# Kernel tuning notes

Measured on AMD Instinct MI355X. Metric: run time of the kernel, lower is better.

## Reference

```python
import jax, jax.numpy as jnp
import numpy as np

B, N, NIN = 32, 128, 64
MSG_HID, MSG_OUT, N_HID, N_OUT = 256, 64, 256, 64
E = N * (N - 1)  # fully connected, no self loops


def setup_inputs() -> dict:
    key = jax.random.key(0)
    ks = jax.random.split(key, 12)

    # one-hot incidence matrices (NRI convention)
    off = np.ones((N, N), dtype=np.float32) - np.eye(N, dtype=np.float32)
    recv_idx, send_idx = np.where(off)
    eye = np.eye(N, dtype=np.float32)
    rel_rec = jnp.asarray(eye[recv_idx])    # [E, N]
    rel_send = jnp.asarray(eye[send_idx])   # [E, N]

    s = 0.05
    inp = {
        "inputs": jax.random.normal(ks[0], (B, N, NIN), jnp.float32),
        "rel_rec": rel_rec,
        "rel_send": rel_send,
        "rel_types": jax.random.uniform(ks[1], (B, E, 2), jnp.float32),
        "msg_fc1_w": jax.random.normal(ks[2], (MSG_HID, 2 * NIN), jnp.float32) * s,
        "msg_fc1_b": jnp.zeros((MSG_HID,), jnp.float32),
        "msg_fc2_w": jax.random.normal(ks[3], (MSG_OUT, MSG_HID), jnp.float32) * s,
        "msg_fc2_b": jnp.zeros((MSG_OUT,), jnp.float32),
        "out_fc1_w": jax.random.normal(ks[4], (N_HID, MSG_OUT), jnp.float32) * s,
        "out_fc1_b": jnp.zeros((N_HID,), jnp.float32),
        "out_fc2_w": jax.random.normal(ks[5], (N_HID, N_HID), jnp.float32) * s,
        "out_fc2_b": jnp.zeros((N_HID,), jnp.float32),
        "out_fc3_w": jax.random.normal(ks[6], (N_OUT, N_HID), jnp.float32) * s,
        "out_fc3_b": jnp.zeros((N_OUT,), jnp.float32),
    }
    return inp


def reference(inputs, rel_rec, rel_send, rel_types,
              msg_fc1_w, msg_fc1_b, msg_fc2_w, msg_fc2_b,
              out_fc1_w, out_fc1_b, out_fc2_w, out_fc2_b,
              out_fc3_w, out_fc3_b):
    # node2edge: gather sender / receiver node features via one-hot matmul
    senders = jnp.einsum('en,bnf->bef', rel_send, inputs)    # [B,E,NIN]
    receivers = jnp.einsum('en,bnf->bef', rel_rec, inputs)   # [B,E,NIN]
    pre_msg = jnp.concatenate([senders, receivers], axis=-1)  # [B,E,2*NIN]

    all_msgs = jnp.zeros(pre_msg.shape[:2] + (MSG_OUT,), pre_msg.dtype)
    for i in range(2):  # edge-type loop (shared weights, as in the original)
        msg = jax.nn.relu(pre_msg @ msg_fc1_w.T + msg_fc1_b)
        msg = jax.nn.relu(msg @ msg_fc2_w.T + msg_fc2_b)
        all_msgs = all_msgs + msg * rel_types[:, :, i:i + 1]

    # edge2node: scatter-add messages to receiving nodes
    agg_msgs = jnp.einsum('bem,en->bnm', all_msgs, rel_rec)   # [B,N,MSG_OUT]

    pred = jax.nn.relu(agg_msgs @ out_fc1_w.T + out_fc1_b)
    pred = jax.nn.relu(pred @ out_fc2_w.T + out_fc2_b)
    pred = pred @ out_fc3_w.T + out_fc3_b                      # [B,N,N_OUT]
    return pred
```

## Files before the change

kernel.cpp:

```cpp
#include <hip/hip_runtime.h>

#define BB 32
#define NN_ 128
#define NIN 64
#define MH 256
#define MO 64
#define NH 256
#define NO 64
#define EDGES 16256

typedef _Float16 half8 __attribute__((ext_vector_type(8)));
typedef _Float16 half2t __attribute__((ext_vector_type(2)));
typedef __attribute__((ext_vector_type(4))) float f32x4;


static __device__ __forceinline__ unsigned short f2h(float f) {
    return __builtin_bit_cast(unsigned short, (_Float16)f);
}

static __device__ __forceinline__ half8 pack8h(float4 f0, float4 f1) {
    uint4 u;
    u.x = __builtin_bit_cast(unsigned, __builtin_amdgcn_cvt_pkrtz(f0.x, f0.y));
    u.y = __builtin_bit_cast(unsigned, __builtin_amdgcn_cvt_pkrtz(f0.z, f0.w));
    u.z = __builtin_bit_cast(unsigned, __builtin_amdgcn_cvt_pkrtz(f1.x, f1.y));
    u.w = __builtin_bit_cast(unsigned, __builtin_amdgcn_cvt_pkrtz(f1.z, f1.w));
    return __builtin_bit_cast(half8, u);
}

static __device__ __forceinline__ half8 addrelu(uint4 s, uint4 p) {
    half8 a = __builtin_bit_cast(half8, s) + __builtin_bit_cast(half8, p);
    half8 z = {};
    return __builtin_elementwise_max(a, z);
}

__global__ __launch_bounds__(256) void prep_kernel(
    const float* __restrict__ x, const float* __restrict__ W1,
    const float* __restrict__ b1, const float* __restrict__ W2,
    const float* __restrict__ O1, const float* __restrict__ O2,
    const float* __restrict__ O3,
    unsigned short* __restrict__ psb, unsigned short* __restrict__ prb,
    unsigned short* __restrict__ w2b, unsigned short* __restrict__ o1b,
    unsigned short* __restrict__ o2b, unsigned short* __restrict__ o3b)
{
    int blk = blockIdx.x;
    int t = threadIdx.x;
    if (blk < 256) {
        int row0 = blk << 4;
        int b = blk >> 3;
        int w = t >> 6, lane = t & 63, ml = lane & 15, q = lane >> 4;

        half8 aX[2];
        #pragma unroll
        for (int s = 0; s < 2; ++s) {
            const float* base = x + (size_t)(row0 + ml) * NIN + s * 32 + q * 8;
            aX[s] = pack8h(*(const float4*)base, *(const float4*)(base + 4));
        }

        #pragma unroll
        for (int half = 0; half < 2; ++half) {
            #pragma unroll
            for (int nt = 0; nt < 4; ++nt) {
                int col = w * 64 + nt * 16 + ml;
                const float* wrow = W1 + (size_t)col * (2 * NIN) + half * 64 + q * 8;
                f32x4 acc = (f32x4){0.f, 0.f, 0.f, 0.f};
                #pragma unroll
                for (int s = 0; s < 2; ++s) {
                    half8 bw = pack8h(*(const float4*)(wrow + 32 * s),
                                      *(const float4*)(wrow + 32 * s + 4));
                    acc = __builtin_amdgcn_mfma_f32_16x16x32_f16(aX[s], bw, acc, 0, 0, 0);
                }
                if (half == 0) {
                    #pragma unroll
                    for (int reg = 0; reg < 4; ++reg) {
                        int n = (row0 + q * 4 + reg) & 127;
                        psb[((size_t)(b * 32 + (col >> 3)) * NN_ + n) * 8 + (col & 7)]
                            = f2h(acc[reg]);
                    }
                } else {
                    float bv = b1[col];
                    #pragma unroll
                    for (int reg = 0; reg < 4; ++reg) {
                        int n = (row0 + q * 4 + reg) & 127;
                        prb[((size_t)(b * NN_) + n) * MH + col] = f2h(acc[reg] + bv);
                    }
                }
            }
        }
    } else if (blk < 320) {
        int i = ((blk - 256) << 8) + t;
        int kc4 = i >> 9, rem = i & 511;
        int n = rem >> 3, k7 = i & 7;
        w2b[i] = f2h(W2[n * MH + kc4 * 8 + k7]);
    } else {
        int i = ((blk - 320) << 8) + t;
        if (i < 16384)       o1b[i]         = f2h(O1[i]);
        else if (i < 81920)  o2b[i - 16384] = f2h(O2[i - 16384]);
        else                 o3b[i - 81920] = f2h(O3[i - 81920]);
    }
}

__global__ __launch_bounds__(256, 3) void edge_kernel(
    const float* __restrict__ rt, const float* __restrict__ b2,
    const unsigned short* __restrict__ psb, const unsigned short* __restrict__ prb,
    const unsigned short* __restrict__ w2b, float* __restrict__ agg)
{
    int blk = blockIdx.x;
    int b = blk >> 6;
    int r0 = (blk & 63) << 1;
    int tid = threadIdx.x;
    int w = tid >> 6, lane = tid & 63, ml = lane & 15, q = lane >> 4;

    __shared__ float rtw_lds[2][128];
    __shared__ float red[2][4][64];
    {
        int rr = tid >> 7, s = tid & 127;
        int r = r0 + rr;
        float v = 0.f;
        if (s != r) {
            int e = r * 127 + s - (s > r ? 1 : 0);
            const float* p = rt + ((size_t)(b * EDGES + e)) * 2;
            v = p[0] + p[1];
        }
        rtw_lds[rr][s] = v;
    }
    __syncthreads();

    int slot0 = 32 * w + ml;
    int slot1 = slot0 + 16;

    const uint4* ps4 = (const uint4*)psb + (size_t)b * (32 * NN_);
    const uint4* pr4_0 = (const uint4*)(prb + ((size_t)(b * NN_ + r0)) * MH);
    const uint4* pr4_1 = (const uint4*)(prb + ((size_t)(b * NN_ + r0 + 1)) * MH);
    const uint4* w24 = (const uint4*)w2b;

    f32x4 acc[2][2][4];
    #pragma unroll
    for (int rr = 0; rr < 2; ++rr)
        #pragma unroll
        for (int mt = 0; mt < 2; ++mt)
            #pragma unroll
            for (int nt = 0; nt < 4; ++nt)
                acc[rr][mt][nt] = (f32x4){0.f, 0.f, 0.f, 0.f};

    #pragma unroll
    for (int kc = 0; kc < 8; ++kc) {
        int kc4 = 4 * kc + q;
        uint4 us0 = ps4[kc4 * NN_ + slot0];
        uint4 us1 = ps4[kc4 * NN_ + slot1];
        uint4 up0 = pr4_0[kc4];
        uint4 up1 = pr4_1[kc4];

        half8 a00 = addrelu(us0, up0);
        half8 a01 = addrelu(us1, up0);
        half8 a10 = addrelu(us0, up1);
        half8 a11 = addrelu(us1, up1);

        #pragma unroll
        for (int nt = 0; nt < 4; ++nt) {
            half8 bw = __builtin_bit_cast(half8, w24[kc4 * 64 + 16 * nt + ml]);
            acc[0][0][nt] = __builtin_amdgcn_mfma_f32_16x16x32_f16(a00, bw, acc[0][0][nt], 0, 0, 0);
            acc[0][1][nt] = __builtin_amdgcn_mfma_f32_16x16x32_f16(a01, bw, acc[0][1][nt], 0, 0, 0);
            acc[1][0][nt] = __builtin_amdgcn_mfma_f32_16x16x32_f16(a10, bw, acc[1][0][nt], 0, 0, 0);
            acc[1][1][nt] = __builtin_amdgcn_mfma_f32_16x16x32_f16(a11, bw, acc[1][1][nt], 0, 0, 0);
        }
    }

    float b2c[4];
    #pragma unroll
    for (int nt = 0; nt < 4; ++nt) b2c[nt] = b2[16 * nt + ml];

    #pragma unroll
    for (int rr = 0; rr < 2; ++rr) {
        float colsum[4] = {0.f, 0.f, 0.f, 0.f};
        #pragma unroll
        for (int mt = 0; mt < 2; ++mt) {
            int slotbase = 32 * w + 16 * mt + 4 * q;
            #pragma unroll
            for (int reg = 0; reg < 4; ++reg) {
                float rw = rtw_lds[rr][slotbase + reg];
                #pragma unroll
                for (int nt = 0; nt < 4; ++nt)
                    colsum[nt] += fmaxf(acc[rr][mt][nt][reg] + b2c[nt], 0.f) * rw;
            }
        }
        #pragma unroll
        for (int nt = 0; nt < 4; ++nt) {
            colsum[nt] += __shfl_xor(colsum[nt], 16);
            colsum[nt] += __shfl_xor(colsum[nt], 32);
        }
        if (lane < 16) {
            #pragma unroll
            for (int nt = 0; nt < 4; ++nt) red[rr][w][16 * nt + ml] = colsum[nt];
        }
    }
    __syncthreads();
    if (tid < 128) {
        int rr = tid >> 6, o = tid & 63;
        agg[((size_t)(b * NN_ + r0 + rr)) * MO + o] =
            red[rr][0][o] + red[rr][1][o] + red[rr][2][o] + red[rr][3][o];
    }
}

__global__ __launch_bounds__(256) void node_kernel(
    const float* __restrict__ agg,
    const unsigned short* __restrict__ O1b, const float* __restrict__ b1o,
    const unsigned short* __restrict__ O2b, const float* __restrict__ b2o,
    const unsigned short* __restrict__ O3b, const float* __restrict__ b3o,
    float* __restrict__ out)
{
    int tid = threadIdx.x;
    int w = tid >> 6, lane = tid & 63, ml = lane & 15, q = lane >> 4;
    int row0 = blockIdx.x << 4;

    __shared__ unsigned short h1L[16][264];
    __shared__ unsigned short h2L[16][264];

    half8 aA[2];
    #pragma unroll
    for (int s = 0; s < 2; ++s) {
        const float* base = agg + (size_t)(row0 + ml) * MO + 32 * s + q * 8;
        aA[s] = pack8h(*(const float4*)base, *(const float4*)(base + 4));
    }

    #pragma unroll
    for (int nt = 0; nt < 4; ++nt) {
        int ntg = w * 4 + nt;
        f32x4 acc = (f32x4){0.f, 0.f, 0.f, 0.f};
        #pragma unroll
        for (int s = 0; s < 2; ++s) {
            half8 bw = *(const half8*)(O1b + (size_t)(ntg * 16 + ml) * 64 + 32 * s + q * 8);
            acc = __builtin_amdgcn_mfma_f32_16x16x32_f16(aA[s], bw, acc, 0, 0, 0);
        }
        float bv = b1o[ntg * 16 + ml];
        #pragma unroll
        for (int reg = 0; reg < 4; ++reg)
            h1L[q * 4 + reg][ntg * 16 + ml] = f2h(fmaxf(acc[reg] + bv, 0.f));
    }
    __syncthreads();

    half8 aH[8];
    #pragma unroll
    for (int ks = 0; ks < 8; ++ks)
        aH[ks] = *(const half8*)&h1L[ml][32 * ks + q * 8];
    #pragma unroll
    for (int nt = 0; nt < 4; ++nt) {
        int ntg = w * 4 + nt;
        const unsigned short* wrow = O2b + (size_t)(ntg * 16 + ml) * NH + q * 8;
        f32x4 acc = (f32x4){0.f, 0.f, 0.f, 0.f};
        #pragma unroll
        for (int ks = 0; ks < 8; ++ks) {
            half8 bw = *(const half8*)(wrow + 32 * ks);
            acc = __builtin_amdgcn_mfma_f32_16x16x32_f16(aH[ks], bw, acc, 0, 0, 0);
        }
        float bv = b2o[ntg * 16 + ml];
        #pragma unroll
        for (int reg = 0; reg < 4; ++reg)
            h2L[q * 4 + reg][ntg * 16 + ml] = f2h(fmaxf(acc[reg] + bv, 0.f));
    }
    __syncthreads();

    #pragma unroll
    for (int ks = 0; ks < 8; ++ks)
        aH[ks] = *(const half8*)&h2L[ml][32 * ks + q * 8];
    {
        const unsigned short* wrow = O3b + (size_t)(w * 16 + ml) * NH + q * 8;
        f32x4 acc = (f32x4){0.f, 0.f, 0.f, 0.f};
        #pragma unroll
        for (int ks = 0; ks < 8; ++ks) {
            half8 bw = *(const half8*)(wrow + 32 * ks);
            acc = __builtin_amdgcn_mfma_f32_16x16x32_f16(aH[ks], bw, acc, 0, 0, 0);
        }
        float bv = b3o[w * 16 + ml];
        #pragma unroll
        for (int reg = 0; reg < 4; ++reg)
            out[(size_t)(row0 + q * 4 + reg) * NO + w * 16 + ml] = acc[reg] + bv;
    }
}

extern "C" void kernel_launch(void* const* d_in, const int* in_sizes, int n_in,
                              void* d_out, int out_size, void* d_ws, size_t ws_size,
                              hipStream_t stream) {
    const float* x   = (const float*)d_in[0];
    const float* rt  = (const float*)d_in[3];
    const float* W1  = (const float*)d_in[4];
    const float* b1  = (const float*)d_in[5];
    const float* W2  = (const float*)d_in[6];
    const float* b2  = (const float*)d_in[7];
    const float* O1  = (const float*)d_in[8];
    const float* b1o = (const float*)d_in[9];
    const float* O2  = (const float*)d_in[10];
    const float* b2o = (const float*)d_in[11];
    const float* O3  = (const float*)d_in[12];
    const float* b3o = (const float*)d_in[13];

    float* ws  = (float*)d_ws;
    unsigned short* psb = (unsigned short*)ws;
    unsigned short* prb = (unsigned short*)(ws + 524288);
    unsigned short* w2b = (unsigned short*)(ws + 1048576);
    float* agg = ws + 1056768;
    unsigned short* o1b = (unsigned short*)(ws + 1318912);
    unsigned short* o2b = (unsigned short*)(ws + 1327104);
    unsigned short* o3b = (unsigned short*)(ws + 1359872);
    float* out = (float*)d_out;

    hipLaunchKernelGGL(prep_kernel, dim3(704), dim3(256), 0, stream,
                       x, W1, b1, W2, O1, O2, O3, psb, prb, w2b, o1b, o2b, o3b);
    hipLaunchKernelGGL(edge_kernel, dim3(2048), dim3(256), 0, stream,
                       rt, b2, psb, prb, w2b, agg);
    hipLaunchKernelGGL(node_kernel, dim3(256), dim3(256), 0, stream,
                       agg, o1b, b1o, o2b, b2o, o3b, b3o, out);
}
```

Baseline: 128.4 us.

## Fuse edge message kernel with node MLP kernel via LDS aggregation

Merges the edge kernel and the node MLP kernel into one launch. Each 512-thread block handles 8 receiver nodes in two teams over two iterations and keeps the aggregated messages in LDS instead of writing them to global memory. It then runs the three-layer node MLP on a zero-padded 16-row tile. This removes one kernel launch and the agg global round trip, but leaves only 512 blocks and wastes half of the node-MLP MFMA work on padding rows.

Result: slower. 256.1 us (+99.5%).

```diff
diff --git a/kernel.cpp b/kernel.cpp
--- a/kernel.cpp
+++ b/kernel.cpp
@@ -10,7 +10,6 @@
 #define EDGES 16256
 
 typedef _Float16 half8 __attribute__((ext_vector_type(8)));
-typedef _Float16 half2t __attribute__((ext_vector_type(2)));
 typedef __attribute__((ext_vector_type(4))) float f32x4;
 
 
@@ -99,136 +98,149 @@
     }
 }
 
-__global__ __launch_bounds__(256, 3) void edge_kernel(
+__global__ __launch_bounds__(512, 4) void edge_node_kernel(
     const float* __restrict__ rt, const float* __restrict__ b2,
     const unsigned short* __restrict__ psb, const unsigned short* __restrict__ prb,
-    const unsigned short* __restrict__ w2b, float* __restrict__ agg)
+    const unsigned short* __restrict__ w2b,
+    const unsigned short* __restrict__ o1b, const float* __restrict__ b1o,
+    const unsigned short* __restrict__ o2b, const float* __restrict__ b2o,
+    const unsigned short* __restrict__ o3b, const float* __restrict__ b3o,
+    float* __restrict__ out)
 {
     int blk = blockIdx.x;
-    int b = blk >> 6;
-    int r0 = (blk & 63) << 1;
-    int tid = threadIdx.x;
-    int w = tid >> 6, lane = tid & 63, ml = lane & 15, q = lane >> 4;
-
-    __shared__ float rtw_lds[2][128];
-    __shared__ float red[2][4][64];
-    {
-        int rr = tid >> 7, s = tid & 127;
-        int r = r0 + rr;
-        float v = 0.f;
-        if (s != r) {
-            int e = r * 127 + s - (s > r ? 1 : 0);
-            const float* p = rt + ((size_t)(b * EDGES + e)) * 2;
-            v = p[0] + p[1];
-        }
-        rtw_lds[rr][s] = v;
-    }
-    __syncthreads();
-
-    int slot0 = 32 * w + ml;
-    int slot1 = slot0 + 16;
+    int t = threadIdx.x;
+    int team = t >> 8;
+    int tl = t & 255;
+    int w = tl >> 6;
+    int lane = t & 63;
+    int ml = lane & 15, q = lane >> 4;
+
+    int b = blk >> 4;
+    int rbase = (blk & 15) << 3;
+
+    __shared__ float rtw_lds[2][2][128];
+    __shared__ float red[2][2][4][64];
+    __shared__ float aggL[16][68];
+    __shared__ unsigned short h1L[16][264];
+    __shared__ unsigned short h2L[16][264];
+
+    aggL[8 + (t >> 6)][lane] = 0.f;
+
+    float b2c[4];
+    #pragma unroll
+    for (int nt = 0; nt < 4; ++nt) b2c[nt] = b2[16 * nt + ml];
 
     const uint4* ps4 = (const uint4*)psb + (size_t)b * (32 * NN_);
-    const uint4* pr4_0 = (const uint4*)(prb + ((size_t)(b * NN_ + r0)) * MH);
-    const uint4* pr4_1 = (const uint4*)(prb + ((size_t)(b * NN_ + r0 + 1)) * MH);
     const uint4* w24 = (const uint4*)w2b;
 
-    f32x4 acc[2][2][4];
-    #pragma unroll
-    for (int rr = 0; rr < 2; ++rr)
-        #pragma unroll
-        for (int mt = 0; mt < 2; ++mt)
-            #pragma unroll
-            for (int nt = 0; nt < 4; ++nt)
-                acc[rr][mt][nt] = (f32x4){0.f, 0.f, 0.f, 0.f};
-
-    #pragma unroll
-    for (int kc = 0; kc < 8; ++kc) {
-        int kc4 = 4 * kc + q;
-        uint4 us0 = ps4[kc4 * NN_ + slot0];
-        uint4 us1 = ps4[kc4 * NN_ + slot1];
-        uint4 up0 = pr4_0[kc4];
-        uint4 up1 = pr4_1[kc4];
-
-        half8 a00 = addrelu(us0, up0);
-        half8 a01 = addrelu(us1, up0);
-        half8 a10 = addrelu(us0, up1);
-        half8 a11 = addrelu(us1, up1);
-
-        #pragma unroll
-        for (int nt = 0; nt < 4; ++nt) {
-            half8 bw = __builtin_bit_cast(half8, w24[kc4 * 64 + 16 * nt + ml]);
-            acc[0][0][nt] = __builtin_amdgcn_mfma_f32_16x16x32_f16(a00, bw, acc[0][0][nt], 0, 0, 0);
-            acc[0][1][nt] = __builtin_amdgcn_mfma_f32_16x16x32_f16(a01, bw, acc[0][1][nt], 0, 0, 0);
-            acc[1][0][nt] = __builtin_amdgcn_mfma_f32_16x16x32_f16(a10, bw, acc[1][0][nt], 0, 0, 0);
-            acc[1][1][nt] = __builtin_amdgcn_mfma_f32_16x16x32_f16(a11, bw, acc[1][1][nt], 0, 0, 0);
-        }
-    }
-
-    float b2c[4];
-    #pragma unroll
-    for (int nt = 0; nt < 4; ++nt) b2c[nt] = b2[16 * nt + ml];
-
-    #pragma unroll
-    for (int rr = 0; rr < 2; ++rr) {
-        float colsum[4] = {0.f, 0.f, 0.f, 0.f};
-        #pragma unroll
-        for (int mt = 0; mt < 2; ++mt) {
-            int slotbase = 32 * w + 16 * mt + 4 * q;
-            #pragma unroll
-            for (int reg = 0; reg < 4; ++reg) {
-                float rw = rtw_lds[rr][slotbase + reg];
+    #pragma unroll 1
+    for (int uu = 0; uu < 2; ++uu) {
+        int lr = uu * 2 + team;
+        int r0 = rbase + lr * 2;
+
+        __syncthreads();
+        {
+            int rr = tl >> 7, s = tl & 127;
+            int r = r0 + rr;
+            float v = 0.f;
+            if (s != r) {
+                int e = r * 127 + s - (s > r ? 1 : 0);
+                const float* p = rt + ((size_t)(b * EDGES + e)) * 2;
+                v = p[0] + p[1];
+            }
+            rtw_lds[team][rr][s] = v;
+        }
+        __syncthreads();
+
+        int slot0 = 32 * w + ml;
+        int slot1 = slot0 + 16;
+
+        const uint4* pr4_0 = (const uint4*)(prb + ((size_t)(b * NN_ + r0)) * MH);
+        const uint4* pr4_1 = (const uint4*)(prb + ((size_t)(b * NN_ + r0 + 1)) * MH);
+
+        f32x4 acc[2][2][4];
+        #pragma unroll
+        for (int rr = 0; rr < 2; ++rr)
+            #pragma unroll
+            for (int mt = 0; mt < 2; ++mt)
                 #pragma unroll
                 for (int nt = 0; nt < 4; ++nt)
-                    colsum[nt] += fmaxf(acc[rr][mt][nt][reg] + b2c[nt], 0.f) * rw;
-            }
-        }
-        #pragma unroll
-        for (int nt = 0; nt < 4; ++nt) {
-            colsum[nt] += __shfl_xor(colsum[nt], 16);
-            colsum[nt] += __shfl_xor(colsum[nt], 32);
-        }
-        if (lane < 16) {
-            #pragma unroll
-            for (int nt = 0; nt < 4; ++nt) red[rr][w][16 * nt + ml] = colsum[nt];
+                    acc[rr][mt][nt] = (f32x4){0.f, 0.f, 0.f, 0.f};
+
+        #pragma unroll
+        for (int kc = 0; kc < 8; ++kc) {
+            int kc4 = 4 * kc + q;
+            uint4 us0 = ps4[kc4 * NN_ + slot0];
+            uint4 us1 = ps4[kc4 * NN_ + slot1];
+            uint4 up0 = pr4_0[kc4];
+            uint4 up1 = pr4_1[kc4];
+
+            half8 a00 = addrelu(us0, up0);
+            half8 a01 = addrelu(us1, up0);
+            half8 a10 = addrelu(us0, up1);
+            half8 a11 = addrelu(us1, up1);
+
+            #pragma unroll
+            for (int nt = 0; nt < 4; ++nt) {
+                half8 bw = __builtin_bit_cast(half8, w24[kc4 * 64 + 16 * nt + ml]);
+                acc[0][0][nt] = __builtin_amdgcn_mfma_f32_16x16x32_f16(a00, bw, acc[0][0][nt], 0, 0, 0);
+                acc[0][1][nt] = __builtin_amdgcn_mfma_f32_16x16x32_f16(a01, bw, acc[0][1][nt], 0, 0, 0);
+                acc[1][0][nt] = __builtin_amdgcn_mfma_f32_16x16x32_f16(a10, bw, acc[1][0][nt], 0, 0, 0);
+                acc[1][1][nt] = __builtin_amdgcn_mfma_f32_16x16x32_f16(a11, bw, acc[1][1][nt], 0, 0, 0);
+            }
+        }
+
+        #pragma unroll
+        for (int rr = 0; rr < 2; ++rr) {
+            float colsum[4] = {0.f, 0.f, 0.f, 0.f};
+            #pragma unroll
+            for (int mt = 0; mt < 2; ++mt) {
+                int slotbase = 32 * w + 16 * mt + 4 * q;
+                #pragma unroll
+                for (int reg = 0; reg < 4; ++reg) {
+                    float rw = rtw_lds[team][rr][slotbase + reg];
+                    #pragma unroll
+                    for (int nt = 0; nt < 4; ++nt)
+                        colsum[nt] += fmaxf(acc[rr][mt][nt][reg] + b2c[nt], 0.f) * rw;
+                }
+            }
+            #pragma unroll
+            for (int nt = 0; nt < 4; ++nt) {
+                colsum[nt] += __shfl_xor(colsum[nt], 16);
+                colsum[nt] += __shfl_xor(colsum[nt], 32);
+            }
+            if (lane < 16) {
+                #pragma unroll
+                for (int nt = 0; nt < 4; ++nt)
+                    red[team][rr][w][16 * nt + ml] = colsum[nt];
+            }
+        }
+        __syncthreads();
+        if (tl < 128) {
+            int rr = tl >> 6, o = tl & 63;
+            aggL[lr * 2 + rr][o] =
+                red[team][rr][0][o] + red[team][rr][1][o] +
+                red[team][rr][2][o] + red[team][rr][3][o];
         }
     }
     __syncthreads();
-    if (tid < 128) {
-        int rr = tid >> 6, o = tid & 63;
-        agg[((size_t)(b * NN_ + r0 + rr)) * MO + o] =
-            red[rr][0][o] + red[rr][1][o] + red[rr][2][o] + red[rr][3][o];
-    }
-}
-
-__global__ __launch_bounds__(256) void node_kernel(
-    const float* __restrict__ agg,
-    const unsigned short* __restrict__ O1b, const float* __restrict__ b1o,
-    const unsigned short* __restrict__ O2b, const float* __restrict__ b2o,
-    const unsigned short* __restrict__ O3b, const float* __restrict__ b3o,
-    float* __restrict__ out)
-{
-    int tid = threadIdx.x;
-    int w = tid >> 6, lane = tid & 63, ml = lane & 15, q = lane >> 4;
-    int row0 = blockIdx.x << 4;
-
-    __shared__ unsigned short h1L[16][264];
-    __shared__ unsigned short h2L[16][264];
+
+    int wv = t >> 6;
 
     half8 aA[2];
     #pragma unroll
     for (int s = 0; s < 2; ++s) {
-        const float* base = agg + (size_t)(row0 + ml) * MO + 32 * s + q * 8;
+        const float* base = &aggL[ml][32 * s + q * 8];
         aA[s] = pack8h(*(const float4*)base, *(const float4*)(base + 4));
     }
 
     #pragma unroll
-    for (int nt = 0; nt < 4; ++nt) {
-        int ntg = w * 4 + nt;
+    for (int nt = 0; nt < 2; ++nt) {
+        int ntg = wv * 2 + nt;
         f32x4 acc = (f32x4){0.f, 0.f, 0.f, 0.f};
         #pragma unroll
         for (int s = 0; s < 2; ++s) {
-            half8 bw = *(const half8*)(O1b + (size_t)(ntg * 16 + ml) * 64 + 32 * s + q * 8);
+            half8 bw = *(const half8*)(o1b + (size_t)(ntg * 16 + ml) * 64 + 32 * s + q * 8);
             acc = __builtin_amdgcn_mfma_f32_16x16x32_f16(aA[s], bw, acc, 0, 0, 0);
         }
         float bv = b1o[ntg * 16 + ml];
@@ -243,9 +255,9 @@
     for (int ks = 0; ks < 8; ++ks)
         aH[ks] = *(const half8*)&h1L[ml][32 * ks + q * 8];
     #pragma unroll
-    for (int nt = 0; nt < 4; ++nt) {
-        int ntg = w * 4 + nt;
-        const unsigned short* wrow = O2b + (size_t)(ntg * 16 + ml) * NH + q * 8;
+    for (int nt = 0; nt < 2; ++nt) {
+        int ntg = wv * 2 + nt;
+        const unsigned short* wrow = o2b + (size_t)(ntg * 16 + ml) * NH + q * 8;
         f32x4 acc = (f32x4){0.f, 0.f, 0.f, 0.f};
         #pragma unroll
         for (int ks = 0; ks < 8; ++ks) {
@@ -259,21 +271,24 @@
     }
     __syncthreads();
 
-    #pragma unroll
-    for (int ks = 0; ks < 8; ++ks)
-        aH[ks] = *(const half8*)&h2L[ml][32 * ks + q * 8];
-    {
-        const unsigned short* wrow = O3b + (size_t)(w * 16 + ml) * NH + q * 8;
+    if (wv < 4) {
+        #pragma unroll
+        for (int ks = 0; ks < 8; ++ks)
+            aH[ks] = *(const half8*)&h2L[ml][32 * ks + q * 8];
+        const unsigned short* wrow = o3b + (size_t)(wv * 16 + ml) * NH + q * 8;
         f32x4 acc = (f32x4){0.f, 0.f, 0.f, 0.f};
         #pragma unroll
         for (int ks = 0; ks < 8; ++ks) {
             half8 bw = *(const half8*)(wrow + 32 * ks);
             acc = __builtin_amdgcn_mfma_f32_16x16x32_f16(aH[ks], bw, acc, 0, 0, 0);
         }
-        float bv = b3o[w * 16 + ml];
-        #pragma unroll
-        for (int reg = 0; reg < 4; ++reg)
-            out[(size_t)(row0 + q * 4 + reg) * NO + w * 16 + ml] = acc[reg] + bv;
+        float bv = b3o[wv * 16 + ml];
+        if (q < 2) {
+            #pragma unroll
+            for (int reg = 0; reg < 4; ++reg)
+                out[(size_t)(b * NN_ + rbase + q * 4 + reg) * NO + wv * 16 + ml]
+                    = acc[reg] + bv;
+        }
     }
 }
 
@@ -297,16 +312,13 @@
     unsigned short* psb = (unsigned short*)ws;
     unsigned short* prb = (unsigned short*)(ws + 524288);
     unsigned short* w2b = (unsigned short*)(ws + 1048576);
-    float* agg = ws + 1056768;
-    unsigned short* o1b = (unsigned short*)(ws + 1318912);
-    unsigned short* o2b = (unsigned short*)(ws + 1327104);
-    unsigned short* o3b = (unsigned short*)(ws + 1359872);
+    unsigned short* o1b = (unsigned short*)(ws + 1056768);
+    unsigned short* o2b = (unsigned short*)(ws + 1064960);
+    unsigned short* o3b = (unsigned short*)(ws + 1097728);
     float* out = (float*)d_out;
 
     hipLaunchKernelGGL(prep_kernel, dim3(704), dim3(256), 0, stream,
                        x, W1, b1, W2, O1, O2, O3, psb, prb, w2b, o1b, o2b, o3b);
-    hipLaunchKernelGGL(edge_kernel, dim3(2048), dim3(256), 0, stream,
-                       rt, b2, psb, prb, w2b, agg);
-    hipLaunchKernelGGL(node_kernel, dim3(256), dim3(256), 0, stream,
-                       agg, o1b, b1o, o2b, b2o, o3b, b3o, out);
-}
+    hipLaunchKernelGGL(edge_node_kernel, dim3(512), dim3(512), 0, stream,
+                       rt, b2, psb, prb, w2b, o1b, b1o, o2b, b2o, o3b, b3o, out);
+}
```
